# Optimization experiments

Hardware: AMD Instinct MI355X
Metric: run time of the kernel (lower is better)

Reference implementation:

```python
import jax, jax.numpy as jnp
import numpy as np

N_NODES = 100000
N_EDGES = 1500000
N_REL = 3
HID = 256


def setup_inputs() -> dict:
    key = jax.random.key(0)
    ks = jax.random.split(key, 8)
    return {
        "feat_a": jax.random.normal(ks[0], (N_NODES, 256), dtype=jnp.float32),
        "feat_b": jax.random.normal(ks[1], (N_NODES, 384), dtype=jnp.float32),
        "Wp_a": jax.random.normal(ks[2], (256, HID), dtype=jnp.float32) * 0.03,
        "Wp_b": jax.random.normal(ks[3], (384, HID), dtype=jnp.float32) * 0.03,
        "Wr": jax.random.normal(ks[4], (N_REL, HID, HID), dtype=jnp.float32) * 0.06,
        "ln_gamma": jnp.ones((HID,), dtype=jnp.float32),
        "ln_beta": jnp.zeros((HID,), dtype=jnp.float32),
        "edge_weight": jax.random.uniform(ks[5], (N_EDGES,), dtype=jnp.float32),
        "edge_src": jax.random.randint(ks[6], (N_EDGES,), 0, N_NODES, dtype=jnp.int32),
        "edge_dst": jax.random.randint(ks[7], (N_EDGES,), 0, N_NODES, dtype=jnp.int32),
    }


def _layer_norm(x, gamma, beta, eps=1e-5):
    mu = jnp.mean(x, axis=-1, keepdims=True)
    var = jnp.mean(jnp.square(x - mu), axis=-1, keepdims=True)
    return (x - mu) * jax.lax.rsqrt(var + eps) * gamma + beta


def reference(feat_a, feat_b, Wp_a, Wp_b, Wr, ln_gamma, ln_beta,
              edge_weight, edge_src, edge_dst):
    # avg fusion of modality projections (bias-free linears), padding node zeroed
    h0 = 0.5 * (feat_a @ Wp_a + feat_b @ Wp_b)  # [N, H]
    h0 = h0.at[0].set(0.0)

    n = h0.shape[0]
    e_per_rel = edge_src.shape[0] // N_REL  # edges pre-sorted by relation id
    aggregated = jnp.zeros_like(h0)
    for r in range(N_REL):
        s = slice(r * e_per_rel, (r + 1) * e_per_rel)
        src, dst, w = edge_src[s], edge_dst[s], edge_weight[s]
        # gather -> relation linear -> weight scale  [E_r, H]
        msg = (h0[src] @ Wr[r]) * w[:, None]
        num = jax.ops.segment_sum(msg, dst, num_segments=n)
        den = jax.ops.segment_sum(w, dst, num_segments=n)
        aggregated = aggregated + num / jnp.maximum(den, 1e-8)[:, None]

    # dropout p=0 / eval -> identity; residual + LayerNorm, padding node zeroed
    h1 = _layer_norm(h0 + aggregated, ln_gamma, ln_beta)
    h1 = h1.at[0].set(0.0)
    return h1
```

## Files before the change

kernel.cpp:

```cpp
#include <hip/hip_runtime.h>

#define N_NODES 100000
#define HID 256
#define N_EDGES 1500000
#define N_REL 3
#define E_PER_REL (N_EDGES / N_REL)
#define NKEYS (N_REL * N_NODES)
#define KP 640
#define KR 768

#define SCAN_CHUNK 1024
#define NSCANBLK ((NKEYS + SCAN_CHUNK - 1) / SCAN_CHUNK)

typedef __attribute__((ext_vector_type(8))) short bf16x8;
typedef __attribute__((ext_vector_type(4))) float f32x4;

__device__ __forceinline__ short f2bf(float x) {
    union { float f; unsigned u; } v; v.f = x;
    unsigned r = v.u + 0x7fffu + ((v.u >> 16) & 1u);
    return (short)(r >> 16);
}
__device__ __forceinline__ float bf2f(short h) {
    union { unsigned u; float f; } v;
    v.u = ((unsigned)(unsigned short)h) << 16;
    return v.f;
}
__device__ __forceinline__ int xorf(int r) { return (r & 3) ^ ((r >> 2) & 3); }

__device__ __forceinline__ void gload16(const void* g, void* l) {
    typedef const __attribute__((address_space(1))) unsigned int gq;
    typedef __attribute__((address_space(3))) unsigned int lq;
    __builtin_amdgcn_global_load_lds((gq*)g, (lq*)l, 16, 0, 0);
}

__global__ __launch_bounds__(256) void wprep_kernel(
    const float* __restrict__ Wa, const float* __restrict__ Wb,
    const float* __restrict__ Wr,
    short* __restrict__ WTp, short* __restrict__ WTr)
{
    int idx = blockIdx.x * 256 + threadIdx.x;
    if (idx < 256 * KP) {
        int c = idx / KP, k = idx - c * KP;
        float v = (k < 256) ? Wa[k * HID + c] : Wb[(k - 256) * HID + c];
        WTp[idx] = f2bf(0.5f * v);
    } else {
        int j = idx - 256 * KP;
        if (j < 256 * KR) {
            int c = j / KR, k = j - c * KR;
            WTr[j] = f2bf(Wr[(k >> 8) * HID * HID + (k & 255) * HID + c]);
        }
    }
}

__global__ __launch_bounds__(512, 2) void proj_gemm(
    const float* __restrict__ fa, const float* __restrict__ fb,
    const short* __restrict__ WTp, short* __restrict__ h0h)
{
    __shared__ alignas(16) char lds[98304];
    const int tid = threadIdx.x;
    const int lane = tid & 63;
    const int w = tid >> 6;
    const int wr = w >> 2, wc = w & 3;
    const int brow = blockIdx.x * 128;

    auto bufA = [&](int b) -> char* { return lds + b * 32768; };
    auto bufB = [&](int b) -> char* { return lds + b * 32768 + 16384; };

    f32x4 acc[4][4] = {};

    const int a_r8 = lane >> 3;
    const int a_sl = (lane & 7) ^ a_r8;
    int aRowG[2];
    #pragma unroll
    for (int ii = 0; ii < 2; ++ii) {
        int i = w * 2 + ii;
        int gr = brow + i * 8 + a_r8;
        aRowG[ii] = (gr < N_NODES) ? gr : (N_NODES - 1);
    }
    const int b_c16 = lane >> 2;
    int bColL[2], bSl[2];
    #pragma unroll
    for (int ii = 0; ii < 2; ++ii) {
        int i = w * 2 + ii;
        bColL[ii] = i * 16 + b_c16;
        bSl[ii] = (lane & 3) ^ xorf(bColL[ii]);
    }

    auto stage = [&](int b, int k0) {
        const float* asrc; int astr, kk;
        if (k0 < 256) { asrc = fa; astr = 256; kk = k0; }
        else          { asrc = fb; astr = 384; kk = k0 - 256; }
        #pragma unroll
        for (int ii = 0; ii < 2; ++ii) {
            int i = w * 2 + ii;
            gload16(asrc + (size_t)aRowG[ii] * astr + kk + a_sl * 4,
                    bufA(b) + i * 1024);
        }
        #pragma unroll
        for (int ii = 0; ii < 2; ++ii) {
            int i = w * 2 + ii;
            gload16(WTp + (size_t)bColL[ii] * KP + k0 + bSl[ii] * 8,
                    bufB(b) + i * 1024);
        }
    };

    const int nt = KP / 32;
    stage(0, 0); stage(1, 32); stage(2, 64);
    int cur = 0;
    for (int t = 0; t < nt; ++t) {
        if (t < nt - 2)       asm volatile("s_waitcnt vmcnt(8)" ::: "memory");
        else if (t == nt - 2) asm volatile("s_waitcnt vmcnt(4)" ::: "memory");
        else                  asm volatile("s_waitcnt vmcnt(0)" ::: "memory");
        __builtin_amdgcn_s_barrier();

        bf16x8 afr[4], bfr[4];
        #pragma unroll
        for (int m = 0; m < 4; ++m) {
            int rt = wr * 64 + m * 16 + (lane & 15);
            int p0 = (((lane >> 4) << 1) | 0) ^ (rt & 7);
            int p1 = (((lane >> 4) << 1) | 1) ^ (rt & 7);
            f32x4 lo = *(const f32x4*)(bufA(cur) + rt * 128 + p0 * 16);
            f32x4 hi = *(const f32x4*)(bufA(cur) + rt * 128 + p1 * 16);
            bf16x8 tb;
            tb[0] = f2bf(lo.x); tb[1] = f2bf(lo.y); tb[2] = f2bf(lo.z); tb[3] = f2bf(lo.w);
            tb[4] = f2bf(hi.x); tb[5] = f2bf(hi.y); tb[6] = f2bf(hi.z); tb[7] = f2bf(hi.w);
            afr[m] = tb;
        }
        #pragma unroll
        for (int n = 0; n < 4; ++n) {
            int ct = wc * 64 + n * 16 + (lane & 15);
            int p = (lane >> 4) ^ xorf(ct);
            bfr[n] = *(const bf16x8*)(bufB(cur) + ct * 64 + p * 16);
        }
        #pragma unroll
        for (int m = 0; m < 4; ++m)
            #pragma unroll
            for (int n = 0; n < 4; ++n)
                acc[m][n] = __builtin_amdgcn_mfma_f32_16x16x32_bf16(
                    afr[m], bfr[n], acc[m][n], 0, 0, 0);

        asm volatile("s_waitcnt lgkmcnt(0)" ::: "memory");
        __builtin_amdgcn_sched_barrier(0);
        __builtin_amdgcn_s_barrier();
        if (t + 3 < nt) stage(cur, (t + 3) * 32);
        cur = (cur == 2) ? 0 : cur + 1;
    }

    #pragma unroll
    for (int m = 0; m < 4; ++m) {
        #pragma unroll
        for (int j = 0; j < 4; ++j) {
            int row = brow + wr * 64 + m * 16 + ((lane >> 4) << 2) + j;
            if (row >= N_NODES) continue;
            #pragma unroll
            for (int n = 0; n < 4; ++n) {
                int col = wc * 64 + n * 16 + (lane & 15);
                short v = (row == 0) ? (short)0 : f2bf(acc[m][n][j]);
                h0h[(size_t)row * HID + col] = v;
            }
        }
    }
}

__global__ __launch_bounds__(512, 4) void rel_gemm_ln(
    const short* __restrict__ S, const short* __restrict__ WTr,
    const short* __restrict__ h0h,
    const float* __restrict__ gamma, const float* __restrict__ beta,
    float* __restrict__ out)
{
    __shared__ alignas(16) char lds[73728];
    const int tid = threadIdx.x;
    const int lane = tid & 63;
    const int w = tid >> 6;
    const int wr = w >> 2, wc = w & 3;
    const int brow = blockIdx.x * 128;

    auto bufA = [&](int b) -> char* { return lds + b * 24576; };
    auto bufB = [&](int b) -> char* { return lds + b * 24576 + 8192; };

    f32x4 acc[4][4] = {};

    const int s_r16 = lane >> 2;
    const int sRowL = w * 16 + s_r16;
    int gr0 = brow + sRowL;
    const int sRowG = (gr0 < N_NODES) ? gr0 : (N_NODES - 1);
    const int sSl = (lane & 3) ^ xorf(sRowL);
    const int b_c16 = lane >> 2;
    int bColL[2], bSl[2];
    #pragma unroll
    for (int ii = 0; ii < 2; ++ii) {
        int i = w * 2 + ii;
        bColL[ii] = i * 16 + b_c16;
        bSl[ii] = (lane & 3) ^ xorf(bColL[ii]);
    }

    auto stage = [&](int b, int k0) {
        gload16(S + (size_t)sRowG * KR + k0 + sSl * 8, bufA(b) + w * 1024);
        #pragma unroll
        for (int ii = 0; ii < 2; ++ii) {
            int i = w * 2 + ii;
            gload16(WTr + (size_t)bColL[ii] * KR + k0 + bSl[ii] * 8,
                    bufB(b) + i * 1024);
        }
    };

    const int nt = KR / 32;
    stage(0, 0); stage(1, 32); stage(2, 64);
    int cur = 0;
    for (int t = 0; t < nt; ++t) {
        if (t < nt - 2)       asm volatile("s_waitcnt vmcnt(6)" ::: "memory");
        else if (t == nt - 2) asm volatile("s_waitcnt vmcnt(3)" ::: "memory");
        else                  asm volatile("s_waitcnt vmcnt(0)" ::: "memory");
        __builtin_amdgcn_s_barrier();

        bf16x8 afr[4], bfr[4];
        #pragma unroll
        for (int m = 0; m < 4; ++m) {
            int rt = wr * 64 + m * 16 + (lane & 15);
            int p = (lane >> 4) ^ xorf(rt);
            afr[m] = *(const bf16x8*)(bufA(cur) + rt * 64 + p * 16);
        }
        #pragma unroll
        for (int n = 0; n < 4; ++n) {
            int ct = wc * 64 + n * 16 + (lane & 15);
            int p = (lane >> 4) ^ xorf(ct);
            bfr[n] = *(const bf16x8*)(bufB(cur) + ct * 64 + p * 16);
        }
        #pragma unroll
        for (int m = 0; m < 4; ++m)
            #pragma unroll
            for (int n = 0; n < 4; ++n)
                acc[m][n] = __builtin_amdgcn_mfma_f32_16x16x32_bf16(
                    afr[m], bfr[n], acc[m][n], 0, 0, 0);

        asm volatile("s_waitcnt lgkmcnt(0)" ::: "memory");
        __builtin_amdgcn_sched_barrier(0);
        __builtin_amdgcn_s_barrier();
        if (t + 3 < nt) stage(cur, (t + 3) * 32);
        cur = (cur == 2) ? 0 : cur + 1;
    }

    float* redS  = (float*)lds;
    float* redS2 = redS + 512;
    float* smMean = redS2 + 512;
    float* smRs   = smMean + 128;

    float gk[4], bk[4];
    #pragma unroll
    for (int n = 0; n < 4; ++n) {
        int col = wc * 64 + n * 16 + (lane & 15);
        gk[n] = gamma[col];
        bk[n] = beta[col];
    }

    #pragma unroll
    for (int m = 0; m < 4; ++m) {
        #pragma unroll
        for (int j = 0; j < 4; ++j) {
            int lrow = wr * 64 + m * 16 + ((lane >> 4) << 2) + j;
            int grow = brow + lrow;
            int crow = (grow < N_NODES) ? grow : 0;
            float s = 0.f, s2 = 0.f;
            #pragma unroll
            for (int n = 0; n < 4; ++n) {
                int col = wc * 64 + n * 16 + (lane & 15);
                float x = acc[m][n][j] + bf2f(h0h[(size_t)crow * HID + col]);
                acc[m][n][j] = x;
                s += x; s2 = fmaf(x, x, s2);
            }
            #pragma unroll
            for (int off = 1; off < 16; off <<= 1) {
                s += __shfl_xor(s, off, 64);
                s2 += __shfl_xor(s2, off, 64);
            }
            if ((lane & 15) == 0) { redS[lrow * 4 + wc] = s; redS2[lrow * 4 + wc] = s2; }
        }
    }
    __syncthreads();
    if (tid < 128) {
        float tot  = redS[tid * 4 + 0] + redS[tid * 4 + 1] + redS[tid * 4 + 2] + redS[tid * 4 + 3];
        float tot2 = redS2[tid * 4 + 0] + redS2[tid * 4 + 1] + redS2[tid * 4 + 2] + redS2[tid * 4 + 3];
        float mean = tot * (1.0f / HID);
        float var = tot2 * (1.0f / HID) - mean * mean;
        smMean[tid] = mean;
        smRs[tid] = rsqrtf(var + 1e-5f);
    }
    __syncthreads();
    #pragma unroll
    for (int m = 0; m < 4; ++m) {
        #pragma unroll
        for (int j = 0; j < 4; ++j) {
            int lrow = wr * 64 + m * 16 + ((lane >> 4) << 2) + j;
            int grow = brow + lrow;
            if (grow >= N_NODES) continue;
            float mean = smMean[lrow], rs = smRs[lrow];
            #pragma unroll
            for (int n = 0; n < 4; ++n) {
                int col = wc * 64 + n * 16 + (lane & 15);
                float y = (acc[m][n][j] - mean) * rs * gk[n] + bk[n];
                out[(size_t)grow * HID + col] = (grow == 0) ? 0.f : y;
            }
        }
    }
}

__global__ __launch_bounds__(256) void hist_kernel(
    const int* __restrict__ dst, int* __restrict__ count)
{
    int i = blockIdx.x * 256 + threadIdx.x;
    if (i >= N_EDGES) return;
    int r = i / E_PER_REL;
    atomicAdd(&count[r * N_NODES + dst[i]], 1);
}

__global__ __launch_bounds__(256) void scan1_kernel(
    const int* __restrict__ count, int* __restrict__ offset,
    int* __restrict__ bsum)
{
    __shared__ int tmp[256];
    const int t = threadIdx.x;
    const int base = blockIdx.x * SCAN_CHUNK + t * 4;
    int v[4];
    #pragma unroll
    for (int j = 0; j < 4; ++j)
        v[j] = (base + j < NKEYS) ? count[base + j] : 0;
    int tsum = v[0] + v[1] + v[2] + v[3];
    tmp[t] = tsum;
    __syncthreads();
    #pragma unroll
    for (int off = 1; off < 256; off <<= 1) {
        int x = (t >= off) ? tmp[t - off] : 0;
        __syncthreads();
        tmp[t] += x;
        __syncthreads();
    }
    int run = tmp[t] - tsum;
    #pragma unroll
    for (int j = 0; j < 4; ++j) {
        if (base + j < NKEYS) offset[base + j] = run;
        run += v[j];
    }
    if (t == 0) bsum[blockIdx.x] = tmp[255];
}

__global__ __launch_bounds__(256) void scan2_kernel(int* __restrict__ bsum)
{
    __shared__ int tmp[256];
    const int t = threadIdx.x;
    int v0 = (2 * t     < NSCANBLK) ? bsum[2 * t]     : 0;
    int v1 = (2 * t + 1 < NSCANBLK) ? bsum[2 * t + 1] : 0;
    int psum = v0 + v1;
    tmp[t] = psum;
    __syncthreads();
    #pragma unroll
    for (int off = 1; off < 256; off <<= 1) {
        int x = (t >= off) ? tmp[t - off] : 0;
        __syncthreads();
        tmp[t] += x;
        __syncthreads();
    }
    int excl = tmp[t] - psum;
    if (2 * t     < NSCANBLK) bsum[2 * t]     = excl;
    if (2 * t + 1 < NSCANBLK) bsum[2 * t + 1] = excl + v0;
}

__global__ __launch_bounds__(256) void scan3_kernel(
    int* __restrict__ offset, const int* __restrict__ bsum)
{
    int i = blockIdx.x * 256 + threadIdx.x;
    if (i >= NKEYS) return;
    offset[i] += bsum[i / SCAN_CHUNK];
}

__global__ __launch_bounds__(256) void fill_kernel(
    const int* __restrict__ src, const int* __restrict__ dst,
    const float* __restrict__ w,
    int* __restrict__ offset, int2* __restrict__ csr_e)
{
    int i = blockIdx.x * 256 + threadIdx.x;
    if (i >= N_EDGES) return;
    int r = i / E_PER_REL;
    int key = r * N_NODES + dst[i];
    int pos = atomicAdd(&offset[key], 1);
    csr_e[pos] = make_int2(src[i], __float_as_int(w[i]));
}

__global__ __launch_bounds__(256) void gather_kernel(
    const short* __restrict__ h0h,
    const int* __restrict__ ends, const int* __restrict__ count,
    const int2* __restrict__ csr_e,
    short* __restrict__ S)
{
    int gw = (blockIdx.x * 256 + threadIdx.x) >> 6;
    int lane = threadIdx.x & 63;
    if (gw >= N_REL * N_NODES) return;
    int r = gw / N_NODES;
    int node = gw - r * N_NODES;
    int deg = count[gw];
    int end = ends[gw];
    int start = end - deg;
    const int colo = lane * 4;

    float a0 = 0.f, a1 = 0.f, a2 = 0.f, a3 = 0.f;
    float den = 0.f;

    if (deg > 0) {
        int degc = (deg < 64) ? deg : 64;
        int2 e = csr_e[start + ((lane < degc) ? lane : 0)];
        int msrc = e.x;
        int mwb = (lane < degc) ? e.y : 0;

        int p = 0;
        for (; p + 4 <= degc; p += 4) {
            #pragma unroll
            for (int j = 0; j < 4; ++j) {
                int q = p + j;
                int sj = __builtin_amdgcn_readlane(msrc, q);
                float wj = __int_as_float(__builtin_amdgcn_readlane(mwb, q));
                const short* rp = h0h + (size_t)sj * HID;
                short4 v = *(const short4*)(rp + colo);
                a0 = fmaf(wj, bf2f(v.x), a0);
                a1 = fmaf(wj, bf2f(v.y), a1);
                a2 = fmaf(wj, bf2f(v.z), a2);
                a3 = fmaf(wj, bf2f(v.w), a3);
                den += wj;
            }
        }
        for (; p < degc; ++p) {
            int sj = __builtin_amdgcn_readlane(msrc, p);
            float wj = __int_as_float(__builtin_amdgcn_readlane(mwb, p));
            const short* rp = h0h + (size_t)sj * HID;
            short4 v = *(const short4*)(rp + colo);
            a0 = fmaf(wj, bf2f(v.x), a0);
            a1 = fmaf(wj, bf2f(v.y), a1);
            a2 = fmaf(wj, bf2f(v.z), a2);
            a3 = fmaf(wj, bf2f(v.w), a3);
            den += wj;
        }
        for (int pp = start + 64; pp < end; ++pp) {
            int2 ee = csr_e[pp];
            float wt = __int_as_float(ee.y);
            short4 v = *(const short4*)(h0h + (size_t)ee.x * HID + colo);
            a0 = fmaf(wt, bf2f(v.x), a0);
            a1 = fmaf(wt, bf2f(v.y), a1);
            a2 = fmaf(wt, bf2f(v.z), a2);
            a3 = fmaf(wt, bf2f(v.w), a3);
            den += wt;
        }
    }

    float inv = 1.0f / fmaxf(den, 1e-8f);
    short4 o;
    o.x = f2bf(a0 * inv);
    o.y = f2bf(a1 * inv);
    o.z = f2bf(a2 * inv);
    o.w = f2bf(a3 * inv);
    *(short4*)(S + (size_t)node * KR + r * HID + colo) = o;
}

extern "C" void kernel_launch(void* const* d_in, const int* in_sizes, int n_in,
                              void* d_out, int out_size, void* d_ws, size_t ws_size,
                              hipStream_t stream) {
    const float* fa    = (const float*)d_in[0];
    const float* fb    = (const float*)d_in[1];
    const float* Wa    = (const float*)d_in[2];
    const float* Wb    = (const float*)d_in[3];
    const float* Wr    = (const float*)d_in[4];
    const float* gamma = (const float*)d_in[5];
    const float* beta  = (const float*)d_in[6];
    const float* ew    = (const float*)d_in[7];
    const int*   esrc  = (const int*)d_in[8];
    const int*   edst  = (const int*)d_in[9];
    float* out = (float*)d_out;

    char* ws = (char*)d_ws;
    size_t off = 0;
    short* h0h     = (short*)(ws + off); off += (size_t)N_NODES * HID * 2;
    short* S       = (short*)(ws + off); off += (size_t)N_NODES * KR * 2;
    short* WTp     = (short*)(ws + off); off += (size_t)256 * KP * 2;
    short* WTr     = (short*)(ws + off); off += (size_t)256 * KR * 2;
    int*   count   = (int*)  (ws + off); off += (size_t)NKEYS * 4;
    int*   offs    = (int*)  (ws + off); off += (size_t)NKEYS * 4;
    int*   bsum    = (int*)  (ws + off); off += 4096;
    int2*  csr_e   = (int2*) (ws + off); off += (size_t)N_EDGES * 8;

    wprep_kernel<<<(256 * KP + 256 * KR) / 256, 256, 0, stream>>>(
        Wa, Wb, Wr, WTp, WTr);

    const int ngrid = (N_NODES + 127) / 128;
    proj_gemm<<<ngrid, 512, 0, stream>>>(fa, fb, WTp, h0h);

    hipMemsetAsync(count, 0, (size_t)NKEYS * 4, stream);
    const int egrid = (N_EDGES + 255) / 256;
    hist_kernel<<<egrid, 256, 0, stream>>>(edst, count);
    scan1_kernel<<<NSCANBLK, 256, 0, stream>>>(count, offs, bsum);
    scan2_kernel<<<1, 256, 0, stream>>>(bsum);
    scan3_kernel<<<(NKEYS + 255) / 256, 256, 0, stream>>>(offs, bsum);
    fill_kernel<<<egrid, 256, 0, stream>>>(esrc, edst, ew, offs, csr_e);

    gather_kernel<<<(N_REL * N_NODES * 64) / 256, 256, 0, stream>>>(
        h0h, offs, count, csr_e, S);

    rel_gemm_ln<<<ngrid, 512, 0, stream>>>(S, WTr, h0h, gamma, beta, out);
}
```

Before: 503.9 us.

## Quantize h0 to per-row int8 for the edge gather, fold scale into edge weights

The projection GEMM epilogue now computes a per-row absmax, writes an int8 copy of h0 plus a per-row scale, and uses packed bf16 conversion instructions for the A operand. The fill kernel folds the source-row scale into a third edge field, widening CSR entries to 16 bytes, and the gather reads 4 bytes of int8 per lane instead of 8 bytes of bf16. The denominator is computed with a wave reduction. This halves gather traffic on the random-access h0 reads, at the cost of int8 precision loss, larger CSR records, and an extra write pass in the GEMM epilogue.

After: 507.5 us. Within noise of the previous version (+0.7%).

```diff
diff --git a/kernel.cpp b/kernel.cpp
--- a/kernel.cpp
+++ b/kernel.cpp
@@ -54,7 +54,8 @@
 
 __global__ __launch_bounds__(512, 2) void proj_gemm(
     const float* __restrict__ fa, const float* __restrict__ fb,
-    const short* __restrict__ WTp, short* __restrict__ h0h)
+    const short* __restrict__ WTp, short* __restrict__ h0h,
+    unsigned char* __restrict__ h0q, float* __restrict__ h0scale)
 {
     __shared__ alignas(16) char lds[98304];
     const int tid = threadIdx.x;
@@ -121,10 +122,12 @@
             int p1 = (((lane >> 4) << 1) | 1) ^ (rt & 7);
             f32x4 lo = *(const f32x4*)(bufA(cur) + rt * 128 + p0 * 16);
             f32x4 hi = *(const f32x4*)(bufA(cur) + rt * 128 + p1 * 16);
-            bf16x8 tb;
-            tb[0] = f2bf(lo.x); tb[1] = f2bf(lo.y); tb[2] = f2bf(lo.z); tb[3] = f2bf(lo.w);
-            tb[4] = f2bf(hi.x); tb[5] = f2bf(hi.y); tb[6] = f2bf(hi.z); tb[7] = f2bf(hi.w);
-            afr[m] = tb;
+            union { bf16x8 h; unsigned u[4]; } cv;
+            asm("v_cvt_pk_bf16_f32 %0, %1, %2" : "=v"(cv.u[0]) : "v"(lo.x), "v"(lo.y));
+            asm("v_cvt_pk_bf16_f32 %0, %1, %2" : "=v"(cv.u[1]) : "v"(lo.z), "v"(lo.w));
+            asm("v_cvt_pk_bf16_f32 %0, %1, %2" : "=v"(cv.u[2]) : "v"(hi.x), "v"(hi.y));
+            asm("v_cvt_pk_bf16_f32 %0, %1, %2" : "=v"(cv.u[3]) : "v"(hi.z), "v"(hi.w));
+            afr[m] = cv.h;
         }
         #pragma unroll
         for (int n = 0; n < 4; ++n) {
@@ -146,17 +149,49 @@
         cur = (cur == 2) ? 0 : cur + 1;
     }
 
+    float* redM  = (float*)lds;
+    float* smInv = redM + 512;
     #pragma unroll
     for (int m = 0; m < 4; ++m) {
         #pragma unroll
         for (int j = 0; j < 4; ++j) {
-            int row = brow + wr * 64 + m * 16 + ((lane >> 4) << 2) + j;
+            int lrow = wr * 64 + m * 16 + ((lane >> 4) << 2) + j;
+            float mx = 0.f;
+            #pragma unroll
+            for (int n = 0; n < 4; ++n) mx = fmaxf(mx, fabsf(acc[m][n][j]));
+            #pragma unroll
+            for (int off = 1; off < 16; off <<= 1)
+                mx = fmaxf(mx, __shfl_xor(mx, off, 64));
+            if ((lane & 15) == 0) redM[lrow * 4 + wc] = mx;
+        }
+    }
+    __syncthreads();
+    if (tid < 128) {
+        float rm = fmaxf(fmaxf(redM[tid * 4 + 0], redM[tid * 4 + 1]),
+                         fmaxf(redM[tid * 4 + 2], redM[tid * 4 + 3]));
+        int grow = brow + tid;
+        smInv[tid] = (rm > 0.f) ? 127.0f / rm : 0.f;
+        if (grow < N_NODES)
+            h0scale[grow] = (grow == 0) ? 0.f : rm * (1.0f / 127.0f);
+    }
+    __syncthreads();
+
+    #pragma unroll
+    for (int m = 0; m < 4; ++m) {
+        #pragma unroll
+        for (int j = 0; j < 4; ++j) {
+            int lrow = wr * 64 + m * 16 + ((lane >> 4) << 2) + j;
+            int row = brow + lrow;
             if (row >= N_NODES) continue;
+            float inv = smInv[lrow];
             #pragma unroll
             for (int n = 0; n < 4; ++n) {
                 int col = wc * 64 + n * 16 + (lane & 15);
-                short v = (row == 0) ? (short)0 : f2bf(acc[m][n][j]);
+                float x = acc[m][n][j];
+                short v = (row == 0) ? (short)0 : f2bf(x);
+                int qi = (row == 0) ? 0 : (int)rintf(x * inv);
                 h0h[(size_t)row * HID + col] = v;
+                h0q[(size_t)row * HID + col] = (unsigned char)(signed char)qi;
             }
         }
     }
@@ -374,21 +409,24 @@
 
 __global__ __launch_bounds__(256) void fill_kernel(
     const int* __restrict__ src, const int* __restrict__ dst,
-    const float* __restrict__ w,
-    int* __restrict__ offset, int2* __restrict__ csr_e)
+    const float* __restrict__ w, const float* __restrict__ h0scale,
+    int* __restrict__ offset, int4* __restrict__ csr4)
 {
     int i = blockIdx.x * 256 + threadIdx.x;
     if (i >= N_EDGES) return;
     int r = i / E_PER_REL;
     int key = r * N_NODES + dst[i];
     int pos = atomicAdd(&offset[key], 1);
-    csr_e[pos] = make_int2(src[i], __float_as_int(w[i]));
+    int s = src[i];
+    float wt = w[i];
+    float ws = wt * h0scale[s];
+    csr4[pos] = make_int4(s, __float_as_int(wt), __float_as_int(ws), 0);
 }
 
 __global__ __launch_bounds__(256) void gather_kernel(
-    const short* __restrict__ h0h,
+    const unsigned char* __restrict__ h0q,
     const int* __restrict__ ends, const int* __restrict__ count,
-    const int2* __restrict__ csr_e,
+    const int4* __restrict__ csr4,
     short* __restrict__ S)
 {
     int gw = (blockIdx.x * 256 + threadIdx.x) >> 6;
@@ -406,9 +444,15 @@
 
     if (deg > 0) {
         int degc = (deg < 64) ? deg : 64;
-        int2 e = csr_e[start + ((lane < degc) ? lane : 0)];
+        int4 e = csr4[start + ((lane < degc) ? lane : 0)];
         int msrc = e.x;
-        int mwb = (lane < degc) ? e.y : 0;
+        float mw = (lane < degc) ? __int_as_float(e.y) : 0.f;
+        int mws = (lane < degc) ? e.z : 0;
+
+        float d = mw;
+        #pragma unroll
+        for (int off = 1; off < 64; off <<= 1) d += __shfl_xor(d, off, 64);
+        den = d;
 
         int p = 0;
         for (; p + 4 <= degc; p += 4) {
@@ -416,35 +460,32 @@
             for (int j = 0; j < 4; ++j) {
                 int q = p + j;
                 int sj = __builtin_amdgcn_readlane(msrc, q);
-                float wj = __int_as_float(__builtin_amdgcn_readlane(mwb, q));
-                const short* rp = h0h + (size_t)sj * HID;
-                short4 v = *(const short4*)(rp + colo);
-                a0 = fmaf(wj, bf2f(v.x), a0);
-                a1 = fmaf(wj, bf2f(v.y), a1);
-                a2 = fmaf(wj, bf2f(v.z), a2);
-                a3 = fmaf(wj, bf2f(v.w), a3);
-                den += wj;
+                float wsj = __int_as_float(__builtin_amdgcn_readlane(mws, q));
+                unsigned qv = *(const unsigned*)(h0q + (size_t)sj * HID + colo);
+                a0 = fmaf(wsj, (float)(int)(signed char)(qv & 255u), a0);
+                a1 = fmaf(wsj, (float)(int)(signed char)((qv >> 8) & 255u), a1);
+                a2 = fmaf(wsj, (float)(int)(signed char)((qv >> 16) & 255u), a2);
+                a3 = fmaf(wsj, (float)(int)(signed char)(qv >> 24), a3);
             }
         }
         for (; p < degc; ++p) {
             int sj = __builtin_amdgcn_readlane(msrc, p);
-            float wj = __int_as_float(__builtin_amdgcn_readlane(mwb, p));
-            const short* rp = h0h + (size_t)sj * HID;
-            short4 v = *(const short4*)(rp + colo);
-            a0 = fmaf(wj, bf2f(v.x), a0);
-            a1 = fmaf(wj, bf2f(v.y), a1);
-            a2 = fmaf(wj, bf2f(v.z), a2);
-            a3 = fmaf(wj, bf2f(v.w), a3);
-            den += wj;
+            float wsj = __int_as_float(__builtin_amdgcn_readlane(mws, p));
+            unsigned qv = *(const unsigned*)(h0q + (size_t)sj * HID + colo);
+            a0 = fmaf(wsj, (float)(int)(signed char)(qv & 255u), a0);
+            a1 = fmaf(wsj, (float)(int)(signed char)((qv >> 8) & 255u), a1);
+            a2 = fmaf(wsj, (float)(int)(signed char)((qv >> 16) & 255u), a2);
+            a3 = fmaf(wsj, (float)(int)(signed char)(qv >> 24), a3);
         }
         for (int pp = start + 64; pp < end; ++pp) {
-            int2 ee = csr_e[pp];
+            int4 ee = csr4[pp];
             float wt = __int_as_float(ee.y);
-            short4 v = *(const short4*)(h0h + (size_t)ee.x * HID + colo);
-            a0 = fmaf(wt, bf2f(v.x), a0);
-            a1 = fmaf(wt, bf2f(v.y), a1);
-            a2 = fmaf(wt, bf2f(v.z), a2);
-            a3 = fmaf(wt, bf2f(v.w), a3);
+            float wsj = __int_as_float(ee.z);
+            unsigned qv = *(const unsigned*)(h0q + (size_t)ee.x * HID + colo);
+            a0 = fmaf(wsj, (float)(int)(signed char)(qv & 255u), a0);
+            a1 = fmaf(wsj, (float)(int)(signed char)((qv >> 8) & 255u), a1);
+            a2 = fmaf(wsj, (float)(int)(signed char)((qv >> 16) & 255u), a2);
+            a3 = fmaf(wsj, (float)(int)(signed char)(qv >> 24), a3);
             den += wt;
         }
     }
@@ -482,13 +523,15 @@
     int*   count   = (int*)  (ws + off); off += (size_t)NKEYS * 4;
     int*   offs    = (int*)  (ws + off); off += (size_t)NKEYS * 4;
     int*   bsum    = (int*)  (ws + off); off += 4096;
-    int2*  csr_e   = (int2*) (ws + off); off += (size_t)N_EDGES * 8;
+    int4*  csr4    = (int4*) (ws + off); off += (size_t)N_EDGES * 16;
+    unsigned char* h0q = (unsigned char*)(ws + off); off += (size_t)N_NODES * HID;
+    float* h0scale = (float*)(ws + off); off += (size_t)N_NODES * 4;
 
     wprep_kernel<<<(256 * KP + 256 * KR) / 256, 256, 0, stream>>>(
         Wa, Wb, Wr, WTp, WTr);
 
     const int ngrid = (N_NODES + 127) / 128;
-    proj_gemm<<<ngrid, 512, 0, stream>>>(fa, fb, WTp, h0h);
+    proj_gemm<<<ngrid, 512, 0, stream>>>(fa, fb, WTp, h0h, h0q, h0scale);
 
     hipMemsetAsync(count, 0, (size_t)NKEYS * 4, stream);
     const int egrid = (N_EDGES + 255) / 256;
@@ -496,10 +539,10 @@
     scan1_kernel<<<NSCANBLK, 256, 0, stream>>>(count, offs, bsum);
     scan2_kernel<<<1, 256, 0, stream>>>(bsum);
     scan3_kernel<<<(NKEYS + 255) / 256, 256, 0, stream>>>(offs, bsum);
-    fill_kernel<<<egrid, 256, 0, stream>>>(esrc, edst, ew, offs, csr_e);
+    fill_kernel<<<egrid, 256, 0, stream>>>(esrc, edst, ew, h0scale, offs, csr4);
 
     gather_kernel<<<(N_REL * N_NODES * 64) / 256, 256, 0, stream>>>(
-        h0h, offs, count, csr_e, S);
+        h0q, offs, count, csr4, S);
 
     rel_gemm_ln<<<ngrid, 512, 0, stream>>>(S, WTr, h0h, gamma, beta, out);
 }
```
